# Performance work log

Hardware: AMD Instinct MI355X
Metric: run time of the kernel (lower is better)

## Reference

```python
import jax, jax.numpy as jnp
import numpy as np

# ---- polar grid config (matches init_kwargs) ----
N_RADIAL = 48
N_ANGULAR = 72
RADIAL_EDGES = jnp.arange(2.0, 51.0, dtype=jnp.float32)            # 49 edges, [2, 50] m
ANGLE_EDGES = jnp.linspace(-np.pi, np.pi, N_ANGULAR + 1).astype(jnp.float32)
Z_MIN, Z_MAX = -3.0, 5.0
MAX_PTS = 64      # max_points_per_voxel
MAX_VOX = 3000    # max_voxels (< H = 3456, truncation path active)
H = N_RADIAL * N_ANGULAR


def setup_inputs() -> dict:
    key = jax.random.key(0)
    pts = jax.random.normal(key, (4_000_000, 5), dtype=jnp.float32)
    # scale xy to ~[-45,45] m and z to ~[-6,6] m so masks keep a realistic fraction
    scale = jnp.array([15.0, 15.0, 2.0, 1.0, 1.0], dtype=jnp.float32)
    return {"points": pts * scale}


def reference(points):
    N, C = points.shape
    x, y, z = points[:, 0], points[:, 1], points[:, 2]
    r = jnp.sqrt(x * x + y * y)
    theta = jnp.arctan2(y, x)

    valid = ((z >= Z_MIN) & (z < Z_MAX)
             & (r >= RADIAL_EDGES[0]) & (r < RADIAL_EDGES[-1])
             & (theta >= ANGLE_EDGES[0]) & (theta < ANGLE_EDGES[-1]))

    # torch.searchsorted(right=False) == jnp side='left'
    r_idx = jnp.clip(jnp.searchsorted(RADIAL_EDGES, r, side='left') - 1, 0, N_RADIAL - 1)
    t_idx = jnp.clip(jnp.searchsorted(ANGLE_EDGES, theta, side='left') - 1, 0, N_ANGULAR - 1)

    # invalid points get sentinel hash H (out of range -> dropped by scatter)
    vhash = jnp.where(valid, r_idx * N_ANGULAR + t_idx, H).astype(jnp.int32)

    # sort points by voxel hash (stable, matching torch.argsort semantics here)
    order = jnp.argsort(vhash)
    sh = vhash[order]                       # [N] sorted hashes
    sp = points[order]                      # [N, C] points in hash order

    # rank of each point within its voxel = position - first occurrence of its hash
    first = jnp.searchsorted(sh, sh, side='left')
    rank = jnp.arange(N, dtype=jnp.int32) - first.astype(jnp.int32)

    # dense hard-voxelization scatter: keep first MAX_PTS points per voxel.
    # out-of-range (sh==H or rank>=MAX_PTS) indices are dropped.
    vox_dense = jnp.zeros((H, MAX_PTS, C), dtype=points.dtype).at[sh, rank].set(sp, mode='drop')

    counts = jax.ops.segment_sum(jnp.ones_like(vhash), vhash, num_segments=H + 1)[:H]
    npts_dense = jnp.minimum(counts, MAX_PTS).astype(jnp.int32)

    # unique occupied hashes in ascending order -> output slots (first MAX_VOX kept)
    occupied = counts > 0
    slot = jnp.cumsum(occupied.astype(jnp.int32)) - 1
    slot = jnp.where(occupied & (slot < MAX_VOX), slot, MAX_VOX)  # MAX_VOX => dropped
    slot2hash = jnp.zeros((MAX_VOX,), jnp.int32).at[slot].set(jnp.arange(H, dtype=jnp.int32), mode='drop')
    slot_valid = jnp.zeros((MAX_VOX,), bool).at[slot].set(True, mode='drop')

    voxels = jnp.where(slot_valid[:, None, None], vox_dense[slot2hash], 0.0)  # [MAX_VOX, MAX_PTS, C]
    num_points = jnp.where(slot_valid, npts_dense[slot2hash], 0)

    ri = slot2hash // N_ANGULAR
    ti = slot2hash % N_ANGULAR
    coords = jnp.where(slot_valid[:, None],
                       jnp.stack([ri, ti, jnp.zeros_like(ri)], axis=1), 0).astype(jnp.int32)

    r_c = 0.5 * (RADIAL_EDGES[ri] + RADIAL_EDGES[ri + 1])
    t_c = 0.5 * (ANGLE_EDGES[ti] + ANGLE_EDGES[ti + 1])
    centers = jnp.where(slot_valid[:, None],
                        jnp.stack([r_c * jnp.cos(t_c), r_c * jnp.sin(t_c)], axis=1), 0.0)

    return voxels, coords, num_points, centers
```

## Files before the change

kernel.cpp:

```cpp
#include <hip/hip_runtime.h>
#include <math.h>

#define NRAD 48
#define NANG 72
#define HV   3456
#define HVW  864
#define MAXP 64
#define MAXV 3000
#define BLK  256
#define CHT  16
#define TILE 4096
#define SUBT 1024
#define NCH  16

#define OFF_C   (MAXV*MAXP*5)
#define OFF_N   (OFF_C + MAXV*3)
#define OFF_X   (OFF_N + MAXV)

#define PI_F 3.14159265358979323846f

__device__ __forceinline__ float angle_edge(int j) {
  const double PI = 3.14159265358979311599796346854;
  const double step = (PI - (-PI)) / 72.0;
  if (j == 72) return (float)PI;
  return (float)(-PI + (double)j * step);
}

__device__ __forceinline__ float next_up_f(float e) {
  if (e == 0.0f) return __uint_as_float(1u);
  unsigned u = __float_as_uint(e);
  u = (e > 0.0f) ? (u + 1u) : (u - 1u);
  return __uint_as_float(u);
}
__device__ __forceinline__ float next_dn_f(float e) {
  if (e == 0.0f) return -__uint_as_float(1u);
  unsigned u = __float_as_uint(e);
  u = (e > 0.0f) ? (u - 1u) : (u + 1u);
  return __uint_as_float(u);
}

__device__ __forceinline__ int point_bin(float x, float y, float z,
                                         const float* __restrict__ ec,
                                         const float* __restrict__ es,
                                         const double* __restrict__ cB,
                                         const double* __restrict__ sB) {
  float r = __fsqrt_rn(__fadd_rn(__fmul_rn(x, x), __fmul_rn(y, y)));
  if (!(z >= -3.0f && z < 5.0f && r >= 2.0f && r < 50.0f)) return HV;
  int ri = (int)ceilf(r) - 3;
  ri = max(0, min(NRAD - 1, ri));
  float ax = fabsf(x), ay = fabsf(y);
  float u = fminf(ax, ay), U = fmaxf(ax, ay);
  bool big = u > 0.41421356f * U;
  float num = big ? (U - u) : u;
  float den = big ? (U + u) : U;
  float v = num * __builtin_amdgcn_rcpf(den);
  float s2 = v * v;
  float pp = v * (1.0f + s2 * (-0.33333333f + s2 * (0.2f - s2 * 0.14285714f)));
  float th1 = big ? (0.78539816f - pp) : pp;
  if (ay > ax) th1 = 1.57079633f - th1;
  if (x < 0.0f) th1 = PI_F - th1;
  float that = copysignf(th1, y);
  int g = (int)floorf((that + PI_F) * 11.459155902616465f);
  g = max(0, min(NANG - 1, g));
  float GA = 2e-6f * r;
  bool unc = false;
  for (;;) {
    float d = __fmaf_rn(ec[g], y, -__fmul_rn(es[g], x));
    if (d > GA) break;
    if (d > -GA || g == 0) { unc = true; break; }
    --g;
  }
  if (!unc) {
    while (g < NANG - 1) {
      float d = __fmaf_rn(ec[g + 1], y, -__fmul_rn(es[g + 1], x));
      if (d < -GA) break;
      if (d <= GA) { unc = true; break; }
      ++g;
    }
    if (!unc && g == NANG - 1) {
      float d = __fmaf_rn(ec[72], y, -__fmul_rn(es[72], x));
      if (d >= -GA) unc = true; else return ri * NANG + g;
    } else if (!unc) {
      return ri * NANG + g;
    }
  }
  double xd = (double)x, yd = (double)y;
  for (;;) {
    if (g == 0) break;
    double d = cB[g] * yd - sB[g] * xd;
    if (d > 0.0) break;
    --g;
  }
  while (g < NANG - 1) {
    double d = cB[g + 1] * yd - sB[g + 1] * xd;
    if (!(d > 0.0)) break;
    ++g;
  }
  if (g == NANG - 1) {
    double d = cB[72] * yd - sB[72] * xd;
    if (d >= 0.0) return HV;
  }
  return ri * NANG + g;
}

__global__ __launch_bounds__(BLK) void k_hist(
    const float* __restrict__ pts, int N, int tile, int n4, int tailN,
    unsigned char* __restrict__ hist, unsigned short* __restrict__ bins,
    float4* __restrict__ out4) {
  __shared__ int lh[HV];
  __shared__ float ec[73], es[73];
  __shared__ double cB[73], sB[73];
  int t = blockIdx.x, tid = threadIdx.x;
  for (int j = t * BLK + tid; j < n4; j += gridDim.x * BLK)
    out4[j] = make_float4(0.f, 0.f, 0.f, 0.f);
  if (t == 0 && tid < tailN) ((float*)out4)[(size_t)n4 * 4 + tid] = 0.f;
  for (int i = tid; i < HV; i += BLK) lh[i] = 0;
  if (tid < 73) {
    float e = angle_edge(tid);
    double ed = (double)e;
    ec[tid] = (float)cos(ed);
    es[tid] = (float)sin(ed);
    double bnd;
    if (tid < 72) bnd = ed + 0.5 * ((double)next_up_f(e) - ed);
    else          bnd = ed - 0.5 * (ed - (double)next_dn_f(e));
    cB[tid] = cos(bnd);
    sB[tid] = sin(bnd);
  }
  __syncthreads();
  int base = t * tile;
  int end  = min(base + tile, N);
  int endq = base + (((end - base) >> 2) << 2);
  const float4* p4 = (const float4*)pts;
  for (int i0 = base + (tid << 2); i0 < endq; i0 += (BLK << 2)) {
    size_t q = (size_t)(i0 >> 2) * 5;
    float4 v0 = p4[q], v1 = p4[q + 1], v2 = p4[q + 2], v3 = p4[q + 3], v4 = p4[q + 4];
    int b0 = point_bin(v0.x, v0.y, v0.z, ec, es, cB, sB);
    int b1 = point_bin(v1.y, v1.z, v1.w, ec, es, cB, sB);
    int b2 = point_bin(v2.z, v2.w, v3.x, ec, es, cB, sB);
    int b3 = point_bin(v3.w, v4.x, v4.y, ec, es, cB, sB);
    *(ushort4*)(bins + i0) = make_ushort4((unsigned short)b0, (unsigned short)b1,
                                          (unsigned short)b2, (unsigned short)b3);
    if (b0 < HV) atomicAdd(&lh[b0], 1);
    if (b1 < HV) atomicAdd(&lh[b1], 1);
    if (b2 < HV) atomicAdd(&lh[b2], 1);
    if (b3 < HV) atomicAdd(&lh[b3], 1);
  }
  for (int i = endq + tid; i < end; i += BLK) {
    size_t p = (size_t)i * 5;
    int b = point_bin(pts[p], pts[p + 1], pts[p + 2], ec, es, cB, sB);
    bins[i] = (unsigned short)b;
    if (b < HV) atomicAdd(&lh[b], 1);
  }
  __syncthreads();
  unsigned char* ht = hist + (size_t)t * HV;
  for (int i = tid; i < HV; i += BLK) ht[i] = (unsigned char)min(lh[i], 64);
}

__global__ void k_scan_a(const unsigned int* __restrict__ hist32, int NT,
                         unsigned int* __restrict__ part32) {
  int w = blockIdx.x * BLK + threadIdx.x;
  int c = blockIdx.y;
  if (w >= HVW) return;
  int t0 = c * CHT, t1 = min(t0 + CHT, NT);
  int s0 = 0, s1 = 0, s2 = 0, s3 = 0;
  for (int t = t0; t < t1; ++t) {
    unsigned int v = hist32[(size_t)t * HVW + w];
    s0 = min(s0 + (int)(v & 255u), 64);
    s1 = min(s1 + (int)((v >> 8) & 255u), 64);
    s2 = min(s2 + (int)((v >> 16) & 255u), 64);
    s3 = min(s3 + (int)(v >> 24), 64);
  }
  part32[(size_t)c * HVW + w] = (unsigned)s0 | ((unsigned)s1 << 8) |
                                ((unsigned)s2 << 16) | ((unsigned)s3 << 24);
}

__global__ __launch_bounds__(1024) void k_scan_cb(
    unsigned int* __restrict__ hist32, int NT, int NC,
    const unsigned int* __restrict__ part32,
    int* __restrict__ soh, float* __restrict__ out) {
  int blk = blockIdx.x;
  int tid = threadIdx.x;
  if (blk < NC) {
    if (tid >= HVW) return;
    int r0 = 0, r1 = 0, r2 = 0, r3 = 0;
    for (int cc = 0; cc < blk; ++cc) {
      unsigned int v = part32[(size_t)cc * HVW + tid];
      r0 = min(r0 + (int)(v & 255u), 64);
      r1 = min(r1 + (int)((v >> 8) & 255u), 64);
      r2 = min(r2 + (int)((v >> 16) & 255u), 64);
      r3 = min(r3 + (int)(v >> 24), 64);
    }
    int t0 = blk * CHT, t1 = min(t0 + CHT, NT);
    for (int t = t0; t < t1; ++t) {
      size_t o = (size_t)t * HVW + tid;
      unsigned int v = hist32[o];
      hist32[o] = (unsigned)r0 | ((unsigned)r1 << 8) |
                  ((unsigned)r2 << 16) | ((unsigned)r3 << 24);
      r0 = min(r0 + (int)(v & 255u), 64);
      r1 = min(r1 + (int)((v >> 8) & 255u), 64);
      r2 = min(r2 + (int)((v >> 16) & 255u), 64);
      r3 = min(r3 + (int)(v >> 24), 64);
    }
  } else {
    __shared__ float eang[73];
    __shared__ int ssum[1024];
    if (tid < 73) eang[tid] = angle_edge(tid);
    int c0 = 0, c1 = 0, c2 = 0, c3 = 0;
    if (tid < HVW) {
      for (int cc = 0; cc < NC; ++cc) {
        unsigned int v = part32[(size_t)cc * HVW + tid];
        c0 = min(c0 + (int)(v & 255u), 64);
        c1 = min(c1 + (int)((v >> 8) & 255u), 64);
        c2 = min(c2 + (int)((v >> 16) & 255u), 64);
        c3 = min(c3 + (int)(v >> 24), 64);
      }
    }
    int occ = (c0 > 0) + (c1 > 0) + (c2 > 0) + (c3 > 0);
    ssum[tid] = occ;
    __syncthreads();
    for (int off = 1; off < 1024; off <<= 1) {
      int v = (tid >= off) ? ssum[tid - off] : 0;
      __syncthreads();
      ssum[tid] += v;
      __syncthreads();
    }
    int base = ssum[tid] - occ;
    if (tid < HVW) {
      int cs[4] = {c0, c1, c2, c3};
#pragma unroll
      for (int k = 0; k < 4; ++k) {
        int h = tid * 4 + k;
        int cnt = cs[k];
        int s = -1;
        if (cnt > 0) {
          if (base < MAXV) s = base;
          base++;
        }
        soh[h] = s;
        if (s >= 0) {
          int ri = h / NANG, ti = h % NANG;
          out[OFF_C + s * 3 + 0] = (float)ri;
          out[OFF_C + s * 3 + 1] = (float)ti;
          out[OFF_C + s * 3 + 2] = 0.0f;
          out[OFF_N + s] = (float)cnt;
          float rc = 2.5f + (float)ri;
          float tc = 0.5f * (eang[ti] + eang[ti + 1]);
          out[OFF_X + s * 2 + 0] = rc * cosf(tc);
          out[OFF_X + s * 2 + 1] = rc * sinf(tc);
        }
      }
    }
  }
}

__global__ __launch_bounds__(BLK) void k_scatter_fast(
    const float* __restrict__ pts, int N,
    const unsigned char* __restrict__ hist, const unsigned short* __restrict__ bins,
    const int* __restrict__ soh, float* __restrict__ out) {
  __shared__ unsigned int whd[4 * HV / 2];
  unsigned short (*wh)[HV] = (unsigned short (*)[HV])whd;
  int t = blockIdx.x;
  int tid = threadIdx.x;
  int lane = tid & 63, wv = tid >> 6;
  for (int i = tid; i < 4 * HV / 2; i += BLK) whd[i] = 0u;
  __syncthreads();
  int base = t * TILE;
  int end  = min(base + TILE, N);
  int sb = base + wv * SUBT;
  int se = min(sb + SUBT, end);
  const unsigned char* ht = hist + (size_t)t * HV;
  unsigned short lb[NCH], lr[NCH];
  const unsigned long long lmask = (1ULL << lane) - 1ULL;
#pragma unroll
  for (int c = 0; c < NCH; ++c) {
    int i = sb + c * 64 + lane;
    int b = 4095;
    if (i < se) {
      int bi = bins[i];
      if (bi < HV && ht[bi] < 64) b = bi;
    }
    lb[c] = (unsigned short)b;
    lr[c] = 0;
    if (__ballot(b != 4095) == 0ULL) continue;
    unsigned long long m = ~0ULL;
#pragma unroll
    for (int k = 0; k < 12; ++k) {
      unsigned long long bal = __ballot((b >> k) & 1);
      m &= ((b >> k) & 1) ? bal : ~bal;
    }
    int rho = __popcll(m & lmask);
    int kap = __popcll(m);
    int cv = 0;
    if (b != 4095) {
      cv = wh[wv][b];
      if (rho == 0) wh[wv][b] = (unsigned short)(cv + kap);
    }
    lr[c] = (unsigned short)(cv + rho);
  }
  __syncthreads();
  for (int j = tid; j < HV; j += BLK) {
    int a0 = wh[0][j], a1 = wh[1][j], a2 = wh[2][j];
    wh[0][j] = 0;
    wh[1][j] = (unsigned short)a0;
    wh[2][j] = (unsigned short)(a0 + a1);
    wh[3][j] = (unsigned short)(a0 + a1 + a2);
  }
  __syncthreads();
#pragma unroll
  for (int c = 0; c < NCH; ++c) {
    int b = lb[c];
    if (b == 4095) continue;
    int rank = (int)ht[b] + (int)wh[wv][b] + (int)lr[c];
    if (rank < MAXP) {
      int s = soh[b];
      if (s >= 0) {
        int i = sb + c * 64 + lane;
        size_t dst = (size_t)(s * MAXP + rank) * 5;
        size_t src = (size_t)i * 5;
        out[dst + 0] = pts[src + 0];
        out[dst + 1] = pts[src + 1];
        out[dst + 2] = pts[src + 2];
        out[dst + 3] = pts[src + 3];
        out[dst + 4] = pts[src + 4];
      }
    }
  }
}

__global__ void k_scatter_gen(const float* __restrict__ pts, int N, int tile,
                              const unsigned char* __restrict__ hist,
                              const unsigned short* __restrict__ bins,
                              const int* __restrict__ soh,
                              float* __restrict__ out) {
  __shared__ int cur[HV + 1];
  int t = blockIdx.x;
  int tid = threadIdx.x;
  const unsigned char* ht = hist + (size_t)t * HV;
  for (int i = tid; i < HV + 1; i += BLK) cur[i] = (i < HV) ? (int)ht[i] : 0;
  __syncthreads();
  int base = t * tile;
  int end  = min(base + tile, N);
  int lane = tid & 63, wv = tid >> 6;
  for (int g = base; g < base + tile; g += BLK) {
    int i = g + tid;
    bool act = (i < end);
    int b = act ? (int)bins[i] : 0x10000;
    int rho = 0, kap = 0;
    for (int j = 0; j < 64; ++j) {
      int bj = __shfl(b, j, 64);
      if (bj == b) { kap++; if (j < lane) rho++; }
    }
    int rank = 0x7FFFFFFF;
    for (int w = 0; w < 4; ++w) {
      if (wv == w && act) {
        int bs = cur[b];
        rank = bs + rho;
        if (rho == 0) cur[b] = bs + kap;
      }
      __syncthreads();
    }
    if (act && rank < MAXP && b < HV) {
      int s = soh[b];
      if (s >= 0) {
        size_t dst = (size_t)(s * MAXP + rank) * 5;
        size_t src = (size_t)i * 5;
        out[dst + 0] = pts[src + 0];
        out[dst + 1] = pts[src + 1];
        out[dst + 2] = pts[src + 2];
        out[dst + 3] = pts[src + 3];
        out[dst + 4] = pts[src + 4];
      }
    }
  }
}

extern "C" void kernel_launch(void* const* d_in, const int* in_sizes, int n_in,
                              void* d_out, int out_size, void* d_ws, size_t ws_size,
                              hipStream_t stream) {
  const float* pts = (const float*)d_in[0];
  int N = in_sizes[0] / 5;
  float* out = (float*)d_out;

  auto align = [](size_t x) { return (x + 255) & ~(size_t)255; };
  int tile = TILE, NT = 1, NC = 1;
  size_t o_hist = 0, o_part = 0, o_soh = 0, o_bins = 0;
  for (;;) {
    NT = (N + tile - 1) / tile;
    NC = (NT + CHT - 1) / CHT;
    o_hist = 0;
    o_part = align(o_hist + (size_t)NT * HV);
    o_soh  = align(o_part + (size_t)NC * HV);
    o_bins = align(o_soh + (size_t)HV * 4);
    size_t need = o_bins + (size_t)N * 2;
    if (need <= ws_size || tile >= (1 << 22)) break;
    tile <<= 1;
  }

  char* w = (char*)d_ws;
  unsigned char* hist = (unsigned char*)(w + o_hist);
  unsigned int*  hist32 = (unsigned int*)hist;
  unsigned int*  part32 = (unsigned int*)(w + o_part);
  int* soh = (int*)(w + o_soh);
  unsigned short* bins = (unsigned short*)(w + o_bins);

  int n4 = out_size / 4;
  int tailN = out_size - n4 * 4;

  k_hist<<<NT, BLK, 0, stream>>>(pts, N, tile, n4, tailN, hist, bins, (float4*)out);
  dim3 ga((HVW + BLK - 1) / BLK, NC);
  k_scan_a<<<ga, BLK, 0, stream>>>(hist32, NT, part32);
  k_scan_cb<<<NC + 1, 1024, 0, stream>>>(hist32, NT, NC, part32, soh, out);
  if (tile == TILE) {
    k_scatter_fast<<<NT, BLK, 0, stream>>>(pts, N, hist, bins, soh, out);
  } else {
    k_scatter_gen<<<NT, BLK, 0, stream>>>(pts, N, tile, hist, bins, soh, out);
  }
}
```

Before: 88.28 us.

## Compute per-tile local ranks in histogram kernel and simplify scatter

Moves the wave-ballot local ranking from the scatter kernel into the histogram kernel, writing a per-point byte rank buffer alongside bins and deriving the tile histogram from the per-wave counts instead of shared atomics. The scatter kernel becomes a simple vectorized stream over bins and ranks with no shared-memory ranking or block syncs. This trades an extra byte-per-point workspace write/read and loses the float4 point loads in the histogram pass.

```diff
diff --git a/kernel.cpp b/kernel.cpp
--- a/kernel.cpp
+++ b/kernel.cpp
@@ -104,6 +104,244 @@
 }
 
 __global__ __launch_bounds__(BLK) void k_hist(
+    const float* __restrict__ pts, int N, int n4, int tailN,
+    unsigned char* __restrict__ hist, unsigned short* __restrict__ bins,
+    unsigned char* __restrict__ lrank, float4* __restrict__ out4) {
+  __shared__ unsigned int whd[4 * HV / 2];
+  unsigned short (*wh)[HV] = (unsigned short (*)[HV])whd;
+  __shared__ float ec[73], es[73];
+  __shared__ double cB[73], sB[73];
+  int t = blockIdx.x, tid = threadIdx.x;
+  int lane = tid & 63, wv = tid >> 6;
+  for (int j = t * BLK + tid; j < n4; j += gridDim.x * BLK)
+    out4[j] = make_float4(0.f, 0.f, 0.f, 0.f);
+  if (t == 0 && tid < tailN) ((float*)out4)[(size_t)n4 * 4 + tid] = 0.f;
+  for (int i = tid; i < 4 * HV / 2; i += BLK) whd[i] = 0u;
+  if (tid < 73) {
+    float e = angle_edge(tid);
+    double ed = (double)e;
+    ec[tid] = (float)cos(ed);
+    es[tid] = (float)sin(ed);
+    double bnd;
+    if (tid < 72) bnd = ed + 0.5 * ((double)next_up_f(e) - ed);
+    else          bnd = ed - 0.5 * (ed - (double)next_dn_f(e));
+    cB[tid] = cos(bnd);
+    sB[tid] = sin(bnd);
+  }
+  __syncthreads();
+  int base = t * TILE;
+  int end  = min(base + TILE, N);
+  int sb = base + wv * SUBT;
+  int se = min(sb + SUBT, end);
+  unsigned short lb[NCH], lr[NCH];
+  const unsigned long long lmask = (1ULL << lane) - 1ULL;
+#pragma unroll
+  for (int c = 0; c < NCH; ++c) {
+    int i = sb + c * 64 + lane;
+    bool act = (i < se);
+    int b = HV;
+    if (act) {
+      size_t p = (size_t)i * 5;
+      b = point_bin(pts[p], pts[p + 1], pts[p + 2], ec, es, cB, sB);
+      bins[i] = (unsigned short)b;
+    }
+    int b2 = (act && b < HV) ? b : 4095;
+    lb[c] = (unsigned short)b2;
+    unsigned long long m = ~0ULL;
+#pragma unroll
+    for (int k = 0; k < 12; ++k) {
+      unsigned long long bal = __ballot((b2 >> k) & 1);
+      m &= ((b2 >> k) & 1) ? bal : ~bal;
+    }
+    int rho = __popcll(m & lmask);
+    int kap = __popcll(m);
+    int cv = 0;
+    if (b2 != 4095) {
+      cv = wh[wv][b2];
+      if (rho == 0) wh[wv][b2] = (unsigned short)(cv + kap);
+    }
+    lr[c] = (unsigned short)(cv + rho);
+  }
+  __syncthreads();
+  unsigned char* ht = hist + (size_t)t * HV;
+  for (int j = tid; j < HV; j += BLK) {
+    int a0 = wh[0][j], a1 = wh[1][j], a2 = wh[2][j], a3 = wh[3][j];
+    wh[0][j] = 0;
+    wh[1][j] = (unsigned short)a0;
+    wh[2][j] = (unsigned short)(a0 + a1);
+    wh[3][j] = (unsigned short)(a0 + a1 + a2);
+    ht[j] = (unsigned char)min(a0 + a1 + a2 + a3, 64);
+  }
+  __syncthreads();
+#pragma unroll
+  for (int c = 0; c < NCH; ++c) {
+    int i = sb + c * 64 + lane;
+    if (i < se) {
+      int b2 = lb[c];
+      lrank[i] = (b2 == 4095) ? 255
+               : (unsigned char)min((int)wh[wv][b2] + (int)lr[c], 255);
+    }
+  }
+}
+
+__global__ void k_scan_a(const unsigned int* __restrict__ hist32, int NT,
+                         unsigned int* __restrict__ part32) {
+  int w = blockIdx.x * BLK + threadIdx.x;
+  int c = blockIdx.y;
+  if (w >= HVW) return;
+  int t0 = c * CHT, t1 = min(t0 + CHT, NT);
+  int s0 = 0, s1 = 0, s2 = 0, s3 = 0;
+  for (int t = t0; t < t1; ++t) {
+    unsigned int v = hist32[(size_t)t * HVW + w];
+    s0 = min(s0 + (int)(v & 255u), 64);
+    s1 = min(s1 + (int)((v >> 8) & 255u), 64);
+    s2 = min(s2 + (int)((v >> 16) & 255u), 64);
+    s3 = min(s3 + (int)(v >> 24), 64);
+  }
+  part32[(size_t)c * HVW + w] = (unsigned)s0 | ((unsigned)s1 << 8) |
+                                ((unsigned)s2 << 16) | ((unsigned)s3 << 24);
+}
+
+__global__ __launch_bounds__(1024) void k_scan_cb(
+    unsigned int* __restrict__ hist32, int NT, int NC,
+    const unsigned int* __restrict__ part32,
+    int* __restrict__ soh, float* __restrict__ out) {
+  int blk = blockIdx.x;
+  int tid = threadIdx.x;
+  if (blk < NC) {
+    if (tid >= HVW) return;
+    int r0 = 0, r1 = 0, r2 = 0, r3 = 0;
+    for (int cc = 0; cc < blk; ++cc) {
+      unsigned int v = part32[(size_t)cc * HVW + tid];
+      r0 = min(r0 + (int)(v & 255u), 64);
+      r1 = min(r1 + (int)((v >> 8) & 255u), 64);
+      r2 = min(r2 + (int)((v >> 16) & 255u), 64);
+      r3 = min(r3 + (int)(v >> 24), 64);
+    }
+    int t0 = blk * CHT, t1 = min(t0 + CHT, NT);
+    for (int t = t0; t < t1; ++t) {
+      size_t o = (size_t)t * HVW + tid;
+      unsigned int v = hist32[o];
+      hist32[o] = (unsigned)r0 | ((unsigned)r1 << 8) |
+                  ((unsigned)r2 << 16) | ((unsigned)r3 << 24);
+      r0 = min(r0 + (int)(v & 255u), 64);
+      r1 = min(r1 + (int)((v >> 8) & 255u), 64);
+      r2 = min(r2 + (int)((v >> 16) & 255u), 64);
+      r3 = min(r3 + (int)(v >> 24), 64);
+    }
+  } else {
+    __shared__ float eang[73];
+    __shared__ int ssum[1024];
+    if (tid < 73) eang[tid] = angle_edge(tid);
+    int c0 = 0, c1 = 0, c2 = 0, c3 = 0;
+    if (tid < HVW) {
+      for (int cc = 0; cc < NC; ++cc) {
+        unsigned int v = part32[(size_t)cc * HVW + tid];
+        c0 = min(c0 + (int)(v & 255u), 64);
+        c1 = min(c1 + (int)((v >> 8) & 255u), 64);
+        c2 = min(c2 + (int)((v >> 16) & 255u), 64);
+        c3 = min(c3 + (int)(v >> 24), 64);
+      }
+    }
+    int occ = (c0 > 0) + (c1 > 0) + (c2 > 0) + (c3 > 0);
+    ssum[tid] = occ;
+    __syncthreads();
+    for (int off = 1; off < 1024; off <<= 1) {
+      int v = (tid >= off) ? ssum[tid - off] : 0;
+      __syncthreads();
+      ssum[tid] += v;
+      __syncthreads();
+    }
+    int base = ssum[tid] - occ;
+    if (tid < HVW) {
+      int cs[4] = {c0, c1, c2, c3};
+#pragma unroll
+      for (int k = 0; k < 4; ++k) {
+        int h = tid * 4 + k;
+        int cnt = cs[k];
+        int s = -1;
+        if (cnt > 0) {
+          if (base < MAXV) s = base;
+          base++;
+        }
+        soh[h] = s;
+        if (s >= 0) {
+          int ri = h / NANG, ti = h % NANG;
+          out[OFF_C + s * 3 + 0] = (float)ri;
+          out[OFF_C + s * 3 + 1] = (float)ti;
+          out[OFF_C + s * 3 + 2] = 0.0f;
+          out[OFF_N + s] = (float)cnt;
+          float rc = 2.5f + (float)ri;
+          float tc = 0.5f * (eang[ti] + eang[ti + 1]);
+          out[OFF_X + s * 2 + 0] = rc * cosf(tc);
+          out[OFF_X + s * 2 + 1] = rc * sinf(tc);
+        }
+      }
+    }
+  }
+}
+
+__global__ __launch_bounds__(BLK) void k_scatter(
+    const float* __restrict__ pts, int N,
+    const unsigned char* __restrict__ hist, const unsigned short* __restrict__ bins,
+    const unsigned char* __restrict__ lrank,
+    const int* __restrict__ soh, float* __restrict__ out) {
+  int t = blockIdx.x, tid = threadIdx.x;
+  int base = t * TILE;
+  int end  = min(base + TILE, N);
+  const unsigned char* ht = hist + (size_t)t * HV;
+#pragma unroll
+  for (int it = 0; it < TILE / (BLK * 4); ++it) {
+    int i0 = base + it * (BLK * 4) + tid * 4;
+    if (i0 >= end) break;
+    if (i0 + 3 < end) {
+      ushort4 bb = *(const ushort4*)(bins + i0);
+      uchar4  ll = *(const uchar4*)(lrank + i0);
+      unsigned short ba[4] = {bb.x, bb.y, bb.z, bb.w};
+      unsigned char  la[4] = {ll.x, ll.y, ll.z, ll.w};
+#pragma unroll
+      for (int k = 0; k < 4; ++k) {
+        int b = ba[k], lr = la[k];
+        if (b < HV && lr < MAXP) {
+          int rank = (int)ht[b] + lr;
+          if (rank < MAXP) {
+            int s = soh[b];
+            if (s >= 0) {
+              size_t dst = (size_t)(s * MAXP + rank) * 5;
+              size_t src = (size_t)(i0 + k) * 5;
+              out[dst + 0] = pts[src + 0];
+              out[dst + 1] = pts[src + 1];
+              out[dst + 2] = pts[src + 2];
+              out[dst + 3] = pts[src + 3];
+              out[dst + 4] = pts[src + 4];
+            }
+          }
+        }
+      }
+    } else {
+      for (int i = i0; i < end; ++i) {
+        int b = bins[i], lr = lrank[i];
+        if (b < HV && lr < MAXP) {
+          int rank = (int)ht[b] + lr;
+          if (rank < MAXP) {
+            int s = soh[b];
+            if (s >= 0) {
+              size_t dst = (size_t)(s * MAXP + rank) * 5;
+              size_t src = (size_t)i * 5;
+              out[dst + 0] = pts[src + 0];
+              out[dst + 1] = pts[src + 1];
+              out[dst + 2] = pts[src + 2];
+              out[dst + 3] = pts[src + 3];
+              out[dst + 4] = pts[src + 4];
+            }
+          }
+        }
+      }
+    }
+  }
+}
+
+__global__ __launch_bounds__(BLK) void k_hist_gen(
     const float* __restrict__ pts, int N, int tile, int n4, int tailN,
     unsigned char* __restrict__ hist, unsigned short* __restrict__ bins,
     float4* __restrict__ out4) {
@@ -129,23 +367,7 @@
   __syncthreads();
   int base = t * tile;
   int end  = min(base + tile, N);
-  int endq = base + (((end - base) >> 2) << 2);
-  const float4* p4 = (const float4*)pts;
-  for (int i0 = base + (tid << 2); i0 < endq; i0 += (BLK << 2)) {
-    size_t q = (size_t)(i0 >> 2) * 5;
-    float4 v0 = p4[q], v1 = p4[q + 1], v2 = p4[q + 2], v3 = p4[q + 3], v4 = p4[q + 4];
-    int b0 = point_bin(v0.x, v0.y, v0.z, ec, es, cB, sB);
-    int b1 = point_bin(v1.y, v1.z, v1.w, ec, es, cB, sB);
-    int b2 = point_bin(v2.z, v2.w, v3.x, ec, es, cB, sB);
-    int b3 = point_bin(v3.w, v4.x, v4.y, ec, es, cB, sB);
-    *(ushort4*)(bins + i0) = make_ushort4((unsigned short)b0, (unsigned short)b1,
-                                          (unsigned short)b2, (unsigned short)b3);
-    if (b0 < HV) atomicAdd(&lh[b0], 1);
-    if (b1 < HV) atomicAdd(&lh[b1], 1);
-    if (b2 < HV) atomicAdd(&lh[b2], 1);
-    if (b3 < HV) atomicAdd(&lh[b3], 1);
-  }
-  for (int i = endq + tid; i < end; i += BLK) {
+  for (int i = base + tid; i < end; i += BLK) {
     size_t p = (size_t)i * 5;
     int b = point_bin(pts[p], pts[p + 1], pts[p + 2], ec, es, cB, sB);
     bins[i] = (unsigned short)b;
@@ -154,177 +376,6 @@
   __syncthreads();
   unsigned char* ht = hist + (size_t)t * HV;
   for (int i = tid; i < HV; i += BLK) ht[i] = (unsigned char)min(lh[i], 64);
-}
-
-__global__ void k_scan_a(const unsigned int* __restrict__ hist32, int NT,
-                         unsigned int* __restrict__ part32) {
-  int w = blockIdx.x * BLK + threadIdx.x;
-  int c = blockIdx.y;
-  if (w >= HVW) return;
-  int t0 = c * CHT, t1 = min(t0 + CHT, NT);
-  int s0 = 0, s1 = 0, s2 = 0, s3 = 0;
-  for (int t = t0; t < t1; ++t) {
-    unsigned int v = hist32[(size_t)t * HVW + w];
-    s0 = min(s0 + (int)(v & 255u), 64);
-    s1 = min(s1 + (int)((v >> 8) & 255u), 64);
-    s2 = min(s2 + (int)((v >> 16) & 255u), 64);
-    s3 = min(s3 + (int)(v >> 24), 64);
-  }
-  part32[(size_t)c * HVW + w] = (unsigned)s0 | ((unsigned)s1 << 8) |
-                                ((unsigned)s2 << 16) | ((unsigned)s3 << 24);
-}
-
-__global__ __launch_bounds__(1024) void k_scan_cb(
-    unsigned int* __restrict__ hist32, int NT, int NC,
-    const unsigned int* __restrict__ part32,
-    int* __restrict__ soh, float* __restrict__ out) {
-  int blk = blockIdx.x;
-  int tid = threadIdx.x;
-  if (blk < NC) {
-    if (tid >= HVW) return;
-    int r0 = 0, r1 = 0, r2 = 0, r3 = 0;
-    for (int cc = 0; cc < blk; ++cc) {
-      unsigned int v = part32[(size_t)cc * HVW + tid];
-      r0 = min(r0 + (int)(v & 255u), 64);
-      r1 = min(r1 + (int)((v >> 8) & 255u), 64);
-      r2 = min(r2 + (int)((v >> 16) & 255u), 64);
-      r3 = min(r3 + (int)(v >> 24), 64);
-    }
-    int t0 = blk * CHT, t1 = min(t0 + CHT, NT);
-    for (int t = t0; t < t1; ++t) {
-      size_t o = (size_t)t * HVW + tid;
-      unsigned int v = hist32[o];
-      hist32[o] = (unsigned)r0 | ((unsigned)r1 << 8) |
-                  ((unsigned)r2 << 16) | ((unsigned)r3 << 24);
-      r0 = min(r0 + (int)(v & 255u), 64);
-      r1 = min(r1 + (int)((v >> 8) & 255u), 64);
-      r2 = min(r2 + (int)((v >> 16) & 255u), 64);
-      r3 = min(r3 + (int)(v >> 24), 64);
-    }
-  } else {
-    __shared__ float eang[73];
-    __shared__ int ssum[1024];
-    if (tid < 73) eang[tid] = angle_edge(tid);
-    int c0 = 0, c1 = 0, c2 = 0, c3 = 0;
-    if (tid < HVW) {
-      for (int cc = 0; cc < NC; ++cc) {
-        unsigned int v = part32[(size_t)cc * HVW + tid];
-        c0 = min(c0 + (int)(v & 255u), 64);
-        c1 = min(c1 + (int)((v >> 8) & 255u), 64);
-        c2 = min(c2 + (int)((v >> 16) & 255u), 64);
-        c3 = min(c3 + (int)(v >> 24), 64);
-      }
-    }
-    int occ = (c0 > 0) + (c1 > 0) + (c2 > 0) + (c3 > 0);
-    ssum[tid] = occ;
-    __syncthreads();
-    for (int off = 1; off < 1024; off <<= 1) {
-      int v = (tid >= off) ? ssum[tid - off] : 0;
-      __syncthreads();
-      ssum[tid] += v;
-      __syncthreads();
-    }
-    int base = ssum[tid] - occ;
-    if (tid < HVW) {
-      int cs[4] = {c0, c1, c2, c3};
-#pragma unroll
-      for (int k = 0; k < 4; ++k) {
-        int h = tid * 4 + k;
-        int cnt = cs[k];
-        int s = -1;
-        if (cnt > 0) {
-          if (base < MAXV) s = base;
-          base++;
-        }
-        soh[h] = s;
-        if (s >= 0) {
-          int ri = h / NANG, ti = h % NANG;
-          out[OFF_C + s * 3 + 0] = (float)ri;
-          out[OFF_C + s * 3 + 1] = (float)ti;
-          out[OFF_C + s * 3 + 2] = 0.0f;
-          out[OFF_N + s] = (float)cnt;
-          float rc = 2.5f + (float)ri;
-          float tc = 0.5f * (eang[ti] + eang[ti + 1]);
-          out[OFF_X + s * 2 + 0] = rc * cosf(tc);
-          out[OFF_X + s * 2 + 1] = rc * sinf(tc);
-        }
-      }
-    }
-  }
-}
-
-__global__ __launch_bounds__(BLK) void k_scatter_fast(
-    const float* __restrict__ pts, int N,
-    const unsigned char* __restrict__ hist, const unsigned short* __restrict__ bins,
-    const int* __restrict__ soh, float* __restrict__ out) {
-  __shared__ unsigned int whd[4 * HV / 2];
-  unsigned short (*wh)[HV] = (unsigned short (*)[HV])whd;
-  int t = blockIdx.x;
-  int tid = threadIdx.x;
-  int lane = tid & 63, wv = tid >> 6;
-  for (int i = tid; i < 4 * HV / 2; i += BLK) whd[i] = 0u;
-  __syncthreads();
-  int base = t * TILE;
-  int end  = min(base + TILE, N);
-  int sb = base + wv * SUBT;
-  int se = min(sb + SUBT, end);
-  const unsigned char* ht = hist + (size_t)t * HV;
-  unsigned short lb[NCH], lr[NCH];
-  const unsigned long long lmask = (1ULL << lane) - 1ULL;
-#pragma unroll
-  for (int c = 0; c < NCH; ++c) {
-    int i = sb + c * 64 + lane;
-    int b = 4095;
-    if (i < se) {
-      int bi = bins[i];
-      if (bi < HV && ht[bi] < 64) b = bi;
-    }
-    lb[c] = (unsigned short)b;
-    lr[c] = 0;
-    if (__ballot(b != 4095) == 0ULL) continue;
-    unsigned long long m = ~0ULL;
-#pragma unroll
-    for (int k = 0; k < 12; ++k) {
-      unsigned long long bal = __ballot((b >> k) & 1);
-      m &= ((b >> k) & 1) ? bal : ~bal;
-    }
-    int rho = __popcll(m & lmask);
-    int kap = __popcll(m);
-    int cv = 0;
-    if (b != 4095) {
-      cv = wh[wv][b];
-      if (rho == 0) wh[wv][b] = (unsigned short)(cv + kap);
-    }
-    lr[c] = (unsigned short)(cv + rho);
-  }
-  __syncthreads();
-  for (int j = tid; j < HV; j += BLK) {
-    int a0 = wh[0][j], a1 = wh[1][j], a2 = wh[2][j];
-    wh[0][j] = 0;
-    wh[1][j] = (unsigned short)a0;
-    wh[2][j] = (unsigned short)(a0 + a1);
-    wh[3][j] = (unsigned short)(a0 + a1 + a2);
-  }
-  __syncthreads();
-#pragma unroll
-  for (int c = 0; c < NCH; ++c) {
-    int b = lb[c];
-    if (b == 4095) continue;
-    int rank = (int)ht[b] + (int)wh[wv][b] + (int)lr[c];
-    if (rank < MAXP) {
-      int s = soh[b];
-      if (s >= 0) {
-        int i = sb + c * 64 + lane;
-        size_t dst = (size_t)(s * MAXP + rank) * 5;
-        size_t src = (size_t)i * 5;
-        out[dst + 0] = pts[src + 0];
-        out[dst + 1] = pts[src + 1];
-        out[dst + 2] = pts[src + 2];
-        out[dst + 3] = pts[src + 3];
-        out[dst + 4] = pts[src + 4];
-      }
-    }
-  }
 }
 
 __global__ void k_scatter_gen(const float* __restrict__ pts, int N, int tile,
@@ -383,7 +434,7 @@
 
   auto align = [](size_t x) { return (x + 255) & ~(size_t)255; };
   int tile = TILE, NT = 1, NC = 1;
-  size_t o_hist = 0, o_part = 0, o_soh = 0, o_bins = 0;
+  size_t o_hist = 0, o_part = 0, o_soh = 0, o_bins = 0, o_lrk = 0;
   for (;;) {
     NT = (N + tile - 1) / tile;
     NC = (NT + CHT - 1) / CHT;
@@ -391,7 +442,8 @@
     o_part = align(o_hist + (size_t)NT * HV);
     o_soh  = align(o_part + (size_t)NC * HV);
     o_bins = align(o_soh + (size_t)HV * 4);
-    size_t need = o_bins + (size_t)N * 2;
+    o_lrk  = align(o_bins + (size_t)N * 2);
+    size_t need = o_lrk + (size_t)N;
     if (need <= ws_size || tile >= (1 << 22)) break;
     tile <<= 1;
   }
@@ -402,16 +454,23 @@
   unsigned int*  part32 = (unsigned int*)(w + o_part);
   int* soh = (int*)(w + o_soh);
   unsigned short* bins = (unsigned short*)(w + o_bins);
+  unsigned char* lrank = (unsigned char*)(w + o_lrk);
 
   int n4 = out_size / 4;
   int tailN = out_size - n4 * 4;
 
-  k_hist<<<NT, BLK, 0, stream>>>(pts, N, tile, n4, tailN, hist, bins, (float4*)out);
+  if (tile == TILE) {
+    k_hist<<<NT, BLK, 0, stream>>>(pts, N, n4, tailN, hist, bins, lrank,
+                                   (float4*)out);
+  } else {
+    k_hist_gen<<<NT, BLK, 0, stream>>>(pts, N, tile, n4, tailN, hist, bins,
+                                       (float4*)out);
+  }
   dim3 ga((HVW + BLK - 1) / BLK, NC);
   k_scan_a<<<ga, BLK, 0, stream>>>(hist32, NT, part32);
   k_scan_cb<<<NC + 1, 1024, 0, stream>>>(hist32, NT, NC, part32, soh, out);
   if (tile == TILE) {
-    k_scatter_fast<<<NT, BLK, 0, stream>>>(pts, N, hist, bins, soh, out);
+    k_scatter<<<NT, BLK, 0, stream>>>(pts, N, hist, bins, lrank, soh, out);
   } else {
     k_scatter_gen<<<NT, BLK, 0, stream>>>(pts, N, tile, hist, bins, soh, out);
   }
```

Measured after the change: 90.05 us. 2.0% more time.
